# Kernel optimization log

Measured on AMD Instinct MI355X. Metric: run time of the kernel, lower is better.

The kernel has to match this reference:

```python
import jax, jax.numpy as jnp
import numpy as np

EPS = 1e-6

def act_quant(x):
    # per-token int8 absmax quantization with straight-through estimator
    scale = 127.0 / jnp.clip(jnp.max(jnp.abs(x), axis=-1, keepdims=True), 1e-5)
    q = jnp.clip(jnp.round(x * scale), -128.0, 127.0) / scale
    return x + jax.lax.stop_gradient(q - x)

def weight_quant(w):
    # ternary absmean quantization with straight-through estimator
    scale = 1.0 / jnp.clip(jnp.mean(jnp.abs(w)), 1e-5)
    q = jnp.clip(jnp.round(w * scale), -1.0, 1.0) / scale
    return w + jax.lax.stop_gradient(q - w)

def bit_linear(x, w):
    # x: [..., in], w: [out, in]
    return jnp.einsum('...i,oi->...o', act_quant(x), weight_quant(w))

def subln(x, g):
    # RMSNorm over last dim with learnable gain
    var = jnp.mean(jnp.square(x), axis=-1, keepdims=True)
    return x * jax.lax.rsqrt(var + EPS) * g

def setup_inputs() -> dict:
    key = jax.random.key(0)
    k1, k2, k3 = jax.random.split(key, 3)
    B, S, H, I = 8, 8192, 512, 2048
    x = jax.random.normal(k1, (B, S, H), dtype=jnp.float32)
    w_up = jax.random.normal(k2, (I, H), dtype=jnp.float32) * (H ** -0.5)
    w_down = jax.random.normal(k3, (H, I), dtype=jnp.float32) * (I ** -0.5)
    g = jnp.ones((I,), dtype=jnp.float32)
    return {'x': x, 'w_up': w_up, 'w_down': w_down, 'g': g}

def reference(x, w_up, w_down, g):
    h = bit_linear(x, w_up)            # [B,S,I]
    h = jnp.square(jax.nn.relu(h))     # relu^2 activation
    h = subln(h, g)                    # SubLN (RMSNorm)
    return bit_linear(h, w_down)       # [B,S,H]
```

## Files before the change

### kernel.cpp

```cpp
#include <hip/hip_runtime.h>
#include <stdint.h>


typedef int v4i __attribute__((ext_vector_type(4)));

#define AS1(p) ((const __attribute__((address_space(1))) void*)(p))
#define AS3(p) ((__attribute__((address_space(3))) void*)(p))

static constexpr size_t OFF_PART = 256;
static constexpr size_t OFF_SX   = 8192;
static constexpr size_t OFF_RSQ  = OFF_SX   + 262144;
static constexpr size_t OFF_S2   = OFF_RSQ  + 262144;
static constexpr size_t OFF_INV2 = OFF_S2   + 262144;
static constexpr size_t OFF_WUQ  = OFF_INV2 + 262144;
static constexpr size_t OFF_WDQ  = OFF_WUQ  + 1048576;
static constexpr size_t OFF_XQ   = OFF_WDQ  + 1048576;
static constexpr size_t OFF_HQ   = OFF_XQ   + 33554432;
static constexpr size_t OFF_SS   = OFF_HQ   + 134217728;
static constexpr size_t OFF_MM   = OFF_SS   + 8388608;

__global__ void wabs_partial(const float* __restrict__ w, double* __restrict__ part)
{
    int t = threadIdx.x, bid = blockIdx.x;
    const float4* w4 = (const float4*)w;
    int base = bid * 256 + t;
    double s = 0.0;
    #pragma unroll
    for (int j = 0; j < 4; ++j) {
        float4 v = w4[base + j * 65536];
        s += (double)fabsf(v.x) + (double)fabsf(v.y)
           + (double)fabsf(v.z) + (double)fabsf(v.w);
    }
    #pragma unroll
    for (int off = 32; off > 0; off >>= 1) s += __shfl_down(s, off);
    __shared__ double ps[4];
    int l = t & 63, wv = t >> 6;
    if (l == 0) ps[wv] = s;
    __syncthreads();
    if (t == 0) part[bid] = ((ps[0] + ps[1]) + ps[2]) + ps[3];
}

__global__ void finalize_sums(const double* __restrict__ part, double* __restrict__ sums)
{
    int t = threadIdx.x;
    double a = part[t];
    double b = part[256 + t];
    #pragma unroll
    for (int off = 32; off > 0; off >>= 1) {
        a += __shfl_down(a, off);
        b += __shfl_down(b, off);
    }
    __shared__ double pa[4], pb[4];
    int l = t & 63, wv = t >> 6;
    if (l == 0) { pa[wv] = a; pb[wv] = b; }
    __syncthreads();
    if (t == 0) {
        sums[0] = ((pa[0] + pa[1]) + pa[2]) + pa[3];
        sums[1] = ((pb[0] + pb[1]) + pb[2]) + pb[3];
    }
}

__global__ void wquant(const float* __restrict__ w, const double* __restrict__ sum,
                       signed char* __restrict__ wq)
{
    int i = blockIdx.x * blockDim.x + threadIdx.x;
    if (i >= 262144) return;
    float mean  = (float)(*sum) * (1.0f / 1048576.0f);
    float scale = 1.0f / fmaxf(mean, 1e-5f);
    float4 v = ((const float4*)w)[i];
    int q0 = (int)fminf(fmaxf(rintf(v.x * scale), -1.f), 1.f);
    int q1 = (int)fminf(fmaxf(rintf(v.y * scale), -1.f), 1.f);
    int q2 = (int)fminf(fmaxf(rintf(v.z * scale), -1.f), 1.f);
    int q3 = (int)fminf(fmaxf(rintf(v.w * scale), -1.f), 1.f);
    unsigned pk = (q0 & 255) | ((q1 & 255) << 8) | ((q2 & 255) << 16) | ((q3 & 255) << 24);
    ((unsigned*)wq)[i] = pk;
}

__global__ void xquant(const float* __restrict__ x, signed char* __restrict__ xq,
                       float* __restrict__ inv_sx)
{
    int row = blockIdx.x * 4 + (threadIdx.x >> 6);
    int l   = threadIdx.x & 63;
    const float* xr = x + (size_t)row * 512;
    float4 v0 = *(const float4*)(xr + l * 8);
    float4 v1 = *(const float4*)(xr + l * 8 + 4);
    float m = fmaxf(fmaxf(fmaxf(fabsf(v0.x), fabsf(v0.y)), fmaxf(fabsf(v0.z), fabsf(v0.w))),
                    fmaxf(fmaxf(fabsf(v1.x), fabsf(v1.y)), fmaxf(fabsf(v1.z), fabsf(v1.w))));
    #pragma unroll
    for (int off = 1; off < 64; off <<= 1) m = fmaxf(m, __shfl_xor(m, off));
    float mc = fmaxf(m, 1e-5f);
    float s  = 127.0f / mc;
    int q[8];
    q[0] = (int)fminf(fmaxf(rintf(v0.x * s), -128.f), 127.f);
    q[1] = (int)fminf(fmaxf(rintf(v0.y * s), -128.f), 127.f);
    q[2] = (int)fminf(fmaxf(rintf(v0.z * s), -128.f), 127.f);
    q[3] = (int)fminf(fmaxf(rintf(v0.w * s), -128.f), 127.f);
    q[4] = (int)fminf(fmaxf(rintf(v1.x * s), -128.f), 127.f);
    q[5] = (int)fminf(fmaxf(rintf(v1.y * s), -128.f), 127.f);
    q[6] = (int)fminf(fmaxf(rintf(v1.z * s), -128.f), 127.f);
    q[7] = (int)fminf(fmaxf(rintf(v1.w * s), -128.f), 127.f);
    uint2 pk;
    pk.x = (q[0] & 255) | ((q[1] & 255) << 8) | ((q[2] & 255) << 16) | ((q[3] & 255) << 24);
    pk.y = (q[4] & 255) | ((q[5] & 255) << 8) | ((q[6] & 255) << 16) | ((q[7] & 255) << 24);
    *(uint2*)(xq + (size_t)row * 512 + l * 8) = pk;
    if (l == 0) inv_sx[row] = mc * (1.0f / 127.0f);
}

__global__ void row_reduce(const float* __restrict__ ss_p, const float* __restrict__ mm_p,
                           float* __restrict__ rsq, float* __restrict__ s2,
                           float* __restrict__ inv2)
{
    int row = blockIdx.x * blockDim.x + threadIdx.x;
    float ss = 0.f, mm = 0.f;
    #pragma unroll
    for (int p = 0; p < 32; ++p) {
        ss += ss_p[(size_t)row * 32 + p];
        mm  = fmaxf(mm, mm_p[(size_t)row * 32 + p]);
    }
    float var  = ss * (1.0f / 2048.0f);
    float r    = 1.0f / sqrtf(var + 1e-6f);
    float maxy = fmaxf(r * mm, 1e-5f);
    rsq[row]  = r;
    s2[row]   = 127.0f / maxy;
    inv2[row] = maxy * (1.0f / 127.0f);
}

template<int K, int N, int EPI>
__global__ __launch_bounds__(256, 2)
void gemm_i8(const signed char* __restrict__ A,
             const signed char* __restrict__ B,
             const float* __restrict__ rowscale,
             const double* __restrict__ wsum,
             const float* __restrict__ g,
             const float* __restrict__ rsq,
             const float* __restrict__ s2,
             float* __restrict__ st_ss,
             float* __restrict__ st_mm,
             signed char* __restrict__ hq,
             float* __restrict__ out)
{
    constexpr int NBN = N / 128;
    __shared__ __align__(16) signed char lA[128 * 64];
    __shared__ __align__(16) signed char lB[128 * 64];

    int nwg  = gridDim.x;
    int orig = blockIdx.x;
    int q8 = nwg >> 3, r8 = nwg & 7;
    int xcd = orig & 7, lin = orig >> 3;
    int swz = (xcd < r8 ? xcd * (q8 + 1) : r8 * (q8 + 1) + (xcd - r8) * q8) + lin;
    int mt = swz / NBN, nt = swz - mt * NBN;

    size_t mbase = (size_t)mt * 128;
    int    nbase = nt * 128;

    int t = threadIdx.x;
    int l = t & 63;
    int wid = t >> 6;
    int wr = wid >> 1, wc = wid & 1;

    v4i acc[4][4] = {};

    const signed char* Ab = A + mbase * K;
    const signed char* Bb = B + (size_t)nbase * K;

    for (int k0 = 0; k0 < K; k0 += 64) {
        #pragma unroll
        for (int i = 0; i < 2; ++i) {
            int lin16 = i * 256 + t;
            int row   = lin16 >> 2;
            int c     = (lin16 & 3) ^ (row & 3);
            __builtin_amdgcn_global_load_lds(AS1(Ab + (size_t)row * K + k0 + c * 16),
                                             AS3(lA + lin16 * 16), 16, 0, 0);
            __builtin_amdgcn_global_load_lds(AS1(Bb + (size_t)row * K + k0 + c * 16),
                                             AS3(lB + lin16 * 16), 16, 0, 0);
        }
        __syncthreads();
        v4i af[4], bf[4];
        #pragma unroll
        for (int r = 0; r < 4; ++r) {
            int arow = wr * 64 + r * 16 + (l & 15);
            int ac   = (l >> 4) ^ (arow & 3);
            af[r] = *reinterpret_cast<const v4i*>(lA + (arow * 4 + ac) * 16);
            int brow = wc * 64 + r * 16 + (l & 15);
            int bc   = (l >> 4) ^ (brow & 3);
            bf[r] = *reinterpret_cast<const v4i*>(lB + (brow * 4 + bc) * 16);
        }
        #pragma unroll
        for (int r = 0; r < 4; ++r)
            #pragma unroll
            for (int c = 0; c < 4; ++c)
                acc[r][c] = __builtin_amdgcn_mfma_i32_16x16x64_i8(af[r], bf[c], acc[r][c], 0, 0, 0);
        __syncthreads();
    }

    float wmean = fmaxf((float)wsum[0] * (1.0f / 1048576.0f), 1e-5f);

    int rsub = wr * 64 + 4 * (l >> 4);
    int csub = wc * 64 + (l & 15);

    if constexpr (EPI == 2) {
        #pragma unroll
        for (int rt = 0; rt < 4; ++rt)
            #pragma unroll
            for (int reg = 0; reg < 4; ++reg) {
                size_t grow = mbase + rsub + rt * 16 + reg;
                float f = rowscale[grow] * wmean;
                #pragma unroll
                for (int ct = 0; ct < 4; ++ct)
                    out[grow * N + nbase + csub + ct * 16] = (float)acc[rt][ct][reg] * f;
            }
    } else {
        float gv[4];
        #pragma unroll
        for (int ct = 0; ct < 4; ++ct) gv[ct] = g[nbase + csub + ct * 16];

        if constexpr (EPI == 0) {
            float ssv[4][4], mmv[4][4];
            #pragma unroll
            for (int rt = 0; rt < 4; ++rt)
                #pragma unroll
                for (int reg = 0; reg < 4; ++reg) {
                    size_t grow = mbase + rsub + rt * 16 + reg;
                    float f = rowscale[grow] * wmean;
                    float ss = 0.f, mm = 0.f;
                    #pragma unroll
                    for (int ct = 0; ct < 4; ++ct) {
                        float z = (float)acc[rt][ct][reg] * f;
                        float a = fmaxf(z, 0.f);
                        float h = a * a;
                        ss += h * h;
                        mm  = fmaxf(mm, fabsf(h * gv[ct]));
                    }
                    ssv[rt][reg] = ss; mmv[rt][reg] = mm;
                }
            #pragma unroll
            for (int off = 1; off < 16; off <<= 1)
                #pragma unroll
                for (int rt = 0; rt < 4; ++rt)
                    #pragma unroll
                    for (int reg = 0; reg < 4; ++reg) {
                        ssv[rt][reg] += __shfl_xor(ssv[rt][reg], off);
                        mmv[rt][reg]  = fmaxf(mmv[rt][reg], __shfl_xor(mmv[rt][reg], off));
                    }
            if ((l & 15) == 0) {
                int p = nt * 2 + wc;
                #pragma unroll
                for (int rt = 0; rt < 4; ++rt)
                    #pragma unroll
                    for (int reg = 0; reg < 4; ++reg) {
                        size_t grow = mbase + rsub + rt * 16 + reg;
                        st_ss[grow * 32 + p] = ssv[rt][reg];
                        st_mm[grow * 32 + p] = mmv[rt][reg];
                    }
            }
        } else {
            #pragma unroll
            for (int rt = 0; rt < 4; ++rt)
                #pragma unroll
                for (int reg = 0; reg < 4; ++reg) {
                    size_t grow = mbase + rsub + rt * 16 + reg;
                    float f  = rowscale[grow] * wmean;
                    float rq = rsq[grow];
                    float sc = s2[grow];
                    #pragma unroll
                    for (int ct = 0; ct < 4; ++ct) {
                        float z = (float)acc[rt][ct][reg] * f;
                        float a = fmaxf(z, 0.f);
                        float h = a * a;
                        float y = (h * rq) * gv[ct];
                        int q = (int)fminf(fmaxf(rintf(y * sc), -128.f), 127.f);
                        hq[grow * 2048 + nbase + csub + ct * 16] = (signed char)q;
                    }
                }
        }
    }
}

extern "C" void kernel_launch(void* const* d_in, const int* in_sizes, int n_in,
                              void* d_out, int out_size, void* d_ws, size_t ws_size,
                              hipStream_t stream)
{
    const float* x  = (const float*)d_in[0];
    const float* wu = (const float*)d_in[1];
    const float* wd = (const float*)d_in[2];
    const float* g  = (const float*)d_in[3];
    float* out = (float*)d_out;
    char*  ws  = (char*)d_ws;

    double* sums     = (double*)ws;
    double* part     = (double*)(ws + OFF_PART);
    float*  inv_sx   = (float*)(ws + OFF_SX);
    float*  rsq      = (float*)(ws + OFF_RSQ);
    float*  s2       = (float*)(ws + OFF_S2);
    float*  inv2     = (float*)(ws + OFF_INV2);
    signed char* wuq = (signed char*)(ws + OFF_WUQ);
    signed char* wdq = (signed char*)(ws + OFF_WDQ);
    signed char* xq  = (signed char*)(ws + OFF_XQ);
    signed char* hq  = (signed char*)(ws + OFF_HQ);
    float*  st_ss    = (float*)(ws + OFF_SS);
    float*  st_mm    = (float*)(ws + OFF_MM);

    wabs_partial<<<256, 256, 0, stream>>>(wu, part);
    wabs_partial<<<256, 256, 0, stream>>>(wd, part + 256);
    finalize_sums<<<1, 256, 0, stream>>>(part, sums);
    wquant<<<1024, 256, 0, stream>>>(wu, sums + 0, wuq);
    wquant<<<1024, 256, 0, stream>>>(wd, sums + 1, wdq);
    xquant<<<16384, 256, 0, stream>>>(x, xq, inv_sx);

    gemm_i8<512, 2048, 0><<<8192, 256, 0, stream>>>(xq, wuq, inv_sx, sums + 0, g,
                                                    nullptr, nullptr, st_ss, st_mm,
                                                    nullptr, nullptr);
    row_reduce<<<256, 256, 0, stream>>>(st_ss, st_mm, rsq, s2, inv2);
    gemm_i8<512, 2048, 1><<<8192, 256, 0, stream>>>(xq, wuq, inv_sx, sums + 0, g,
                                                    rsq, s2, nullptr, nullptr,
                                                    hq, nullptr);
    gemm_i8<2048, 512, 2><<<2048, 256, 0, stream>>>(hq, wdq, inv2, sums + 1,
                                                    nullptr, nullptr, nullptr,
                                                    nullptr, nullptr, nullptr, out);
}
```

Measured before the change: 552.2 us.

## Rewrite int8 GEMM with 256x256 tiles, 8 waves and double-buffered LDS pipeline

The int8 GEMM moves from 128x128 tiles with 4 waves and a single-buffered 64-wide K step to 256x256 tiles with 8 waves and 128-wide K tiles. The K tiles sit in a double-buffered LDS ping-pong split into four phases. Each phase issues async global-to-LDS loads for a later K tile while its MFMAs run, using explicit barriers, vmcnt waits and setprio. The goal is to hide global load latency and raise operand reuse per byte loaded, at the cost of a 128KB LDS footprint, higher register pressure and fewer workgroups per launch.

```diff
diff --git a/kernel.cpp b/kernel.cpp
--- a/kernel.cpp
+++ b/kernel.cpp
@@ -125,8 +125,69 @@
     inv2[row] = maxy * (1.0f / 127.0f);
 }
 
+
+#define PHASE(MH, NH, STAGE_STMT, TAIL_STMT)                                   \
+  {                                                                            \
+    v4i af[8]; v4i bf[4];                                                      \
+    _Pragma("unroll")                                                          \
+    for (int mm = 0; mm < 4; ++mm) {                                           \
+      _Pragma("unroll")                                                        \
+      for (int ks = 0; ks < 2; ++ks) {                                         \
+        int r  = wr * 128 + ((MH) * 4 + mm) * 16 + lr;                         \
+        int eg = (ks * 4 + lg) ^ lx;                                           \
+        af[mm * 2 + ks] = *(const v4i*)(Ab + r * 128 + eg * 16);               \
+      }                                                                        \
+    }                                                                          \
+    _Pragma("unroll")                                                          \
+    for (int nn = 0; nn < 2; ++nn) {                                           \
+      _Pragma("unroll")                                                        \
+      for (int ks = 0; ks < 2; ++ks) {                                         \
+        int r  = wc * 64 + ((NH) * 2 + nn) * 16 + lr;                          \
+        int eg = (ks * 4 + lg) ^ lx;                                           \
+        bf[nn * 2 + ks] = *(const v4i*)(Bb + r * 128 + eg * 16);               \
+      }                                                                        \
+    }                                                                          \
+    STAGE_STMT;                                                                \
+    __builtin_amdgcn_s_barrier();                                              \
+    asm volatile("s_waitcnt lgkmcnt(0)" ::: "memory");                         \
+    __builtin_amdgcn_sched_barrier(0);                                         \
+    __builtin_amdgcn_s_setprio(1);                                             \
+    _Pragma("unroll")                                                          \
+    for (int mm = 0; mm < 4; ++mm)                                             \
+      _Pragma("unroll")                                                        \
+      for (int nn = 0; nn < 2; ++nn)                                           \
+        _Pragma("unroll")                                                      \
+        for (int ks = 0; ks < 2; ++ks)                                         \
+          acc[(MH) * 4 + mm][(NH) * 2 + nn] =                                  \
+              __builtin_amdgcn_mfma_i32_16x16x64_i8(                           \
+                  af[mm * 2 + ks], bf[nn * 2 + ks],                            \
+                  acc[(MH) * 4 + mm][(NH) * 2 + nn], 0, 0, 0);                 \
+    __builtin_amdgcn_s_setprio(0);                                             \
+    TAIL_STMT;                                                                 \
+    __builtin_amdgcn_s_barrier();                                              \
+  }
+
+#define KTILE(KT, P)                                                           \
+  {                                                                            \
+    const char* Ab = &lds[P][0][0];                                            \
+    const char* Bb = &lds[P][1][0];                                            \
+    const int kt_ = (KT);                                                      \
+    PHASE(0, 0, { if (kt_ + 1 < NKT) stageA((P) ^ 1, 1, kt_ + 1); }, {})       \
+    PHASE(0, 1, { if (kt_ + 1 < NKT) stageB((P) ^ 1, 1, kt_ + 1); }, {})       \
+    PHASE(1, 0, { if (kt_ + 2 < NKT) stageA((P), 0, kt_ + 2); }, {})           \
+    PHASE(1, 1, { if (kt_ + 2 < NKT) stageB((P), 0, kt_ + 2); },               \
+          {                                                                    \
+            if (kt_ < NKT - 1) {                                               \
+              if (kt_ + 2 < NKT)                                               \
+                asm volatile("s_waitcnt vmcnt(4)" ::: "memory");               \
+              else                                                             \
+                asm volatile("s_waitcnt vmcnt(0)" ::: "memory");               \
+            }                                                                  \
+          })                                                                   \
+  }
+
 template<int K, int N, int EPI>
-__global__ __launch_bounds__(256, 2)
+__global__ __launch_bounds__(512, 2)
 void gemm_i8(const signed char* __restrict__ A,
              const signed char* __restrict__ B,
              const float* __restrict__ rowscale,
@@ -139,9 +200,9 @@
              signed char* __restrict__ hq,
              float* __restrict__ out)
 {
-    constexpr int NBN = N / 128;
-    __shared__ __align__(16) signed char lA[128 * 64];
-    __shared__ __align__(16) signed char lB[128 * 64];
+    constexpr int NKT = K / 128;
+    constexpr int NBN = N / 256;
+    __shared__ __align__(16) char lds[2][2][32768];
 
     int nwg  = gridDim.x;
     int orig = blockIdx.x;
@@ -150,126 +211,124 @@
     int swz = (xcd < r8 ? xcd * (q8 + 1) : r8 * (q8 + 1) + (xcd - r8) * q8) + lin;
     int mt = swz / NBN, nt = swz - mt * NBN;
 
-    size_t mbase = (size_t)mt * 128;
-    int    nbase = nt * 128;
-
-    int t = threadIdx.x;
-    int l = t & 63;
+    size_t mbase = (size_t)mt * 256;
+    int    nbase = nt * 256;
+
+    int t  = threadIdx.x;
+    int l  = t & 63;
     int wid = t >> 6;
-    int wr = wid >> 1, wc = wid & 1;
-
-    v4i acc[4][4] = {};
-
-    const signed char* Ab = A + mbase * K;
-    const signed char* Bb = B + (size_t)nbase * K;
-
-    for (int k0 = 0; k0 < K; k0 += 64) {
+    int wr = wid >> 2, wc = wid & 3;
+    int lr = l & 15, lg = l >> 4, lx = l & 7;
+
+    const signed char* Ag = A + mbase * K;
+    const signed char* Bg = B + (size_t)nbase * K;
+
+    auto stageA = [&](int buf, int sel, int ktt) {
+        char* d0 = &lds[buf][0][0];
         #pragma unroll
         for (int i = 0; i < 2; ++i) {
-            int lin16 = i * 256 + t;
-            int row   = lin16 >> 2;
-            int c     = (lin16 & 3) ^ (row & 3);
-            __builtin_amdgcn_global_load_lds(AS1(Ab + (size_t)row * K + k0 + c * 16),
-                                             AS3(lA + lin16 * 16), 16, 0, 0);
-            __builtin_amdgcn_global_load_lds(AS1(Bb + (size_t)row * K + k0 + c * 16),
-                                             AS3(lB + lin16 * 16), 16, 0, 0);
+            int j = i * 512 + t;
+            int rho = j >> 3, gg = j & 7;
+            int r = rho + (rho & 64) + sel * 64;
+            int kg = gg ^ (r & 7);
+            __builtin_amdgcn_global_load_lds(AS1(Ag + (size_t)r * K + ktt * 128 + kg * 16),
+                                             AS3(d0 + r * 128 + gg * 16), 16, 0, 0);
         }
-        __syncthreads();
-        v4i af[4], bf[4];
+    };
+    auto stageB = [&](int buf, int sel, int ktt) {
+        char* d0 = &lds[buf][1][0];
         #pragma unroll
-        for (int r = 0; r < 4; ++r) {
-            int arow = wr * 64 + r * 16 + (l & 15);
-            int ac   = (l >> 4) ^ (arow & 3);
-            af[r] = *reinterpret_cast<const v4i*>(lA + (arow * 4 + ac) * 16);
-            int brow = wc * 64 + r * 16 + (l & 15);
-            int bc   = (l >> 4) ^ (brow & 3);
-            bf[r] = *reinterpret_cast<const v4i*>(lB + (brow * 4 + bc) * 16);
+        for (int i = 0; i < 2; ++i) {
+            int j = i * 512 + t;
+            int rho = j >> 3, gg = j & 7;
+            int r = ((rho & ~31) << 1) + (rho & 31) + sel * 32;
+            int kg = gg ^ (r & 7);
+            __builtin_amdgcn_global_load_lds(AS1(Bg + (size_t)r * K + ktt * 128 + kg * 16),
+                                             AS3(d0 + r * 128 + gg * 16), 16, 0, 0);
         }
-        #pragma unroll
-        for (int r = 0; r < 4; ++r)
-            #pragma unroll
-            for (int c = 0; c < 4; ++c)
-                acc[r][c] = __builtin_amdgcn_mfma_i32_16x16x64_i8(af[r], bf[c], acc[r][c], 0, 0, 0);
-        __syncthreads();
+    };
+
+    v4i acc[8][4] = {};
+
+    stageA(0, 0, 0); stageB(0, 0, 0); stageA(0, 1, 0); stageB(0, 1, 0);
+    if (NKT > 1) {
+        stageA(1, 0, 1); stageB(1, 0, 1);
+        asm volatile("s_waitcnt vmcnt(4)" ::: "memory");
+    } else {
+        asm volatile("s_waitcnt vmcnt(0)" ::: "memory");
+    }
+    __builtin_amdgcn_s_barrier();
+
+    #pragma unroll 1
+    for (int kt2 = 0; kt2 < NKT / 2; ++kt2) {
+        int kt = kt2 * 2;
+        KTILE(kt, 0)
+        KTILE(kt + 1, 1)
     }
 
     float wmean = fmaxf((float)wsum[0] * (1.0f / 1048576.0f), 1e-5f);
-
-    int rsub = wr * 64 + 4 * (l >> 4);
-    int csub = wc * 64 + (l & 15);
+    size_t rowb = mbase + (size_t)wr * 128;
+    int    colb = nbase + wc * 64;
 
     if constexpr (EPI == 2) {
         #pragma unroll
-        for (int rt = 0; rt < 4; ++rt)
+        for (int m = 0; m < 8; ++m)
             #pragma unroll
             for (int reg = 0; reg < 4; ++reg) {
-                size_t grow = mbase + rsub + rt * 16 + reg;
+                size_t grow = rowb + m * 16 + lg * 4 + reg;
                 float f = rowscale[grow] * wmean;
                 #pragma unroll
-                for (int ct = 0; ct < 4; ++ct)
-                    out[grow * N + nbase + csub + ct * 16] = (float)acc[rt][ct][reg] * f;
+                for (int n = 0; n < 4; ++n)
+                    out[grow * N + colb + n * 16 + lr] = (float)acc[m][n][reg] * f;
             }
     } else {
         float gv[4];
         #pragma unroll
-        for (int ct = 0; ct < 4; ++ct) gv[ct] = g[nbase + csub + ct * 16];
+        for (int n = 0; n < 4; ++n) gv[n] = g[colb + n * 16 + lr];
 
         if constexpr (EPI == 0) {
-            float ssv[4][4], mmv[4][4];
             #pragma unroll
-            for (int rt = 0; rt < 4; ++rt)
+            for (int m = 0; m < 8; ++m)
                 #pragma unroll
                 for (int reg = 0; reg < 4; ++reg) {
-                    size_t grow = mbase + rsub + rt * 16 + reg;
+                    size_t grow = rowb + m * 16 + lg * 4 + reg;
                     float f = rowscale[grow] * wmean;
-                    float ss = 0.f, mm = 0.f;
+                    float ss = 0.f, mx = 0.f;
                     #pragma unroll
-                    for (int ct = 0; ct < 4; ++ct) {
-                        float z = (float)acc[rt][ct][reg] * f;
+                    for (int n = 0; n < 4; ++n) {
+                        float z = (float)acc[m][n][reg] * f;
                         float a = fmaxf(z, 0.f);
                         float h = a * a;
                         ss += h * h;
-                        mm  = fmaxf(mm, fabsf(h * gv[ct]));
+                        mx  = fmaxf(mx, fabsf(h * gv[n]));
                     }
-                    ssv[rt][reg] = ss; mmv[rt][reg] = mm;
+                    #pragma unroll
+                    for (int off = 1; off < 16; off <<= 1) {
+                        ss += __shfl_xor(ss, off);
+                        mx  = fmaxf(mx, __shfl_xor(mx, off));
+                    }
+                    if (lr == 0) {
+                        st_ss[grow * 32 + nt * 4 + wc] = ss;
+                        st_mm[grow * 32 + nt * 4 + wc] = mx;
+                    }
                 }
-            #pragma unroll
-            for (int off = 1; off < 16; off <<= 1)
-                #pragma unroll
-                for (int rt = 0; rt < 4; ++rt)
-                    #pragma unroll
-                    for (int reg = 0; reg < 4; ++reg) {
-                        ssv[rt][reg] += __shfl_xor(ssv[rt][reg], off);
-                        mmv[rt][reg]  = fmaxf(mmv[rt][reg], __shfl_xor(mmv[rt][reg], off));
-                    }
-            if ((l & 15) == 0) {
-                int p = nt * 2 + wc;
-                #pragma unroll
-                for (int rt = 0; rt < 4; ++rt)
-                    #pragma unroll
-                    for (int reg = 0; reg < 4; ++reg) {
-                        size_t grow = mbase + rsub + rt * 16 + reg;
-                        st_ss[grow * 32 + p] = ssv[rt][reg];
-                        st_mm[grow * 32 + p] = mmv[rt][reg];
-                    }
-            }
         } else {
             #pragma unroll
-            for (int rt = 0; rt < 4; ++rt)
+            for (int m = 0; m < 8; ++m)
                 #pragma unroll
                 for (int reg = 0; reg < 4; ++reg) {
-                    size_t grow = mbase + rsub + rt * 16 + reg;
+                    size_t grow = rowb + m * 16 + lg * 4 + reg;
                     float f  = rowscale[grow] * wmean;
                     float rq = rsq[grow];
                     float sc = s2[grow];
                     #pragma unroll
-                    for (int ct = 0; ct < 4; ++ct) {
-                        float z = (float)acc[rt][ct][reg] * f;
+                    for (int n = 0; n < 4; ++n) {
+                        float z = (float)acc[m][n][reg] * f;
                         float a = fmaxf(z, 0.f);
                         float h = a * a;
-                        float y = (h * rq) * gv[ct];
-                        int q = (int)fminf(fmaxf(rintf(y * sc), -128.f), 127.f);
-                        hq[grow * 2048 + nbase + csub + ct * 16] = (signed char)q;
+                        float y = (h * rq) * gv[n];
+                        int qv = (int)fminf(fmaxf(rintf(y * sc), -128.f), 127.f);
+                        hq[grow * 2048 + colb + n * 16 + lr] = (signed char)qv;
                     }
                 }
         }
@@ -307,14 +366,14 @@
     wquant<<<1024, 256, 0, stream>>>(wd, sums + 1, wdq);
     xquant<<<16384, 256, 0, stream>>>(x, xq, inv_sx);
 
-    gemm_i8<512, 2048, 0><<<8192, 256, 0, stream>>>(xq, wuq, inv_sx, sums + 0, g,
+    gemm_i8<512, 2048, 0><<<2048, 512, 0, stream>>>(xq, wuq, inv_sx, sums + 0, g,
                                                     nullptr, nullptr, st_ss, st_mm,
                                                     nullptr, nullptr);
     row_reduce<<<256, 256, 0, stream>>>(st_ss, st_mm, rsq, s2, inv2);
-    gemm_i8<512, 2048, 1><<<8192, 256, 0, stream>>>(xq, wuq, inv_sx, sums + 0, g,
+    gemm_i8<512, 2048, 1><<<2048, 512, 0, stream>>>(xq, wuq, inv_sx, sums + 0, g,
                                                     rsq, s2, nullptr, nullptr,
                                                     hq, nullptr);
-    gemm_i8<2048, 512, 2><<<2048, 256, 0, stream>>>(hq, wdq, inv2, sums + 1,
-                                                    nullptr, nullptr, nullptr,
-                                                    nullptr, nullptr, nullptr, out);
-}
+    gemm_i8<2048, 512, 2><<<512, 512, 0, stream>>>(hq, wdq, inv2, sums + 1,
+                                                   nullptr, nullptr, nullptr,
+                                                   nullptr, nullptr, nullptr, out);
+}
```

After: 597.2 us. 1.08x slower.

## Replace recomputed up-projection GEMM with int16 staging and a row norm-quant kernel

Applied to the files above, without the earlier changes.

The up-projection GEMM now runs once and stores raw integer accumulators as int16 through an LDS-staged, vectorized write. A new per-row kernel applies the scale, relu², RMS norm and int8 quantization. Before, the GEMM was run twice: once to gather row statistics and once to quantize. The pipeline is processed in four row chunks so the int16 intermediate has a chance to stay in the last-level cache between kernels. The LDS swizzle is also adjusted. Truncating int32 accumulators to int16 can overflow for inputs with large accumulated sums, which adds a correctness risk.

```diff
diff --git a/kernel.cpp b/kernel.cpp
--- a/kernel.cpp
+++ b/kernel.cpp
@@ -7,17 +7,15 @@
 #define AS1(p) ((const __attribute__((address_space(1))) void*)(p))
 #define AS3(p) ((__attribute__((address_space(3))) void*)(p))
 
+static constexpr int CHUNK = 16384;
 static constexpr size_t OFF_PART = 256;
 static constexpr size_t OFF_SX   = 8192;
-static constexpr size_t OFF_RSQ  = OFF_SX   + 262144;
-static constexpr size_t OFF_S2   = OFF_RSQ  + 262144;
-static constexpr size_t OFF_INV2 = OFF_S2   + 262144;
+static constexpr size_t OFF_INV2 = OFF_SX   + 262144;
 static constexpr size_t OFF_WUQ  = OFF_INV2 + 262144;
 static constexpr size_t OFF_WDQ  = OFF_WUQ  + 1048576;
 static constexpr size_t OFF_XQ   = OFF_WDQ  + 1048576;
-static constexpr size_t OFF_HQ   = OFF_XQ   + 33554432;
-static constexpr size_t OFF_SS   = OFF_HQ   + 134217728;
-static constexpr size_t OFF_MM   = OFF_SS   + 8388608;
+static constexpr size_t OFF_Z16  = OFF_XQ   + 33554432;
+static constexpr size_t OFF_HQ   = OFF_Z16  + 67108864;
 
 __global__ void wabs_partial(const float* __restrict__ w, double* __restrict__ part)
 {
@@ -106,23 +104,60 @@
     if (l == 0) inv_sx[row] = mc * (1.0f / 127.0f);
 }
 
-__global__ void row_reduce(const float* __restrict__ ss_p, const float* __restrict__ mm_p,
-                           float* __restrict__ rsq, float* __restrict__ s2,
-                           float* __restrict__ inv2)
-{
-    int row = blockIdx.x * blockDim.x + threadIdx.x;
+__global__ __launch_bounds__(256)
+void norm_quant(const short* __restrict__ z16, const float* __restrict__ inv_sx,
+                const double* __restrict__ wsum, const float* __restrict__ g,
+                signed char* __restrict__ hq, float* __restrict__ inv2)
+{
+    int row = blockIdx.x;
+    int t = threadIdx.x;
+    float wmean = fmaxf((float)wsum[0] * (1.0f / 1048576.0f), 1e-5f);
+    float f = inv_sx[row] * wmean;
+
+    v4i zi = *(const v4i*)(z16 + (size_t)row * 2048 + t * 8);
+    const short* zs = (const short*)&zi;
+    float4 g0 = *(const float4*)(g + t * 8);
+    float4 g1 = *(const float4*)(g + t * 8 + 4);
+    float gv[8] = {g0.x, g0.y, g0.z, g0.w, g1.x, g1.y, g1.z, g1.w};
+
+    float h[8];
     float ss = 0.f, mm = 0.f;
     #pragma unroll
-    for (int p = 0; p < 32; ++p) {
-        ss += ss_p[(size_t)row * 32 + p];
-        mm  = fmaxf(mm, mm_p[(size_t)row * 32 + p]);
-    }
-    float var  = ss * (1.0f / 2048.0f);
+    for (int j = 0; j < 8; ++j) {
+        float z = (float)zs[j] * f;
+        float a = fmaxf(z, 0.f);
+        h[j] = a * a;
+        ss += h[j] * h[j];
+        mm  = fmaxf(mm, fabsf(h[j] * gv[j]));
+    }
+    #pragma unroll
+    for (int off = 1; off < 64; off <<= 1) {
+        ss += __shfl_xor(ss, off);
+        mm  = fmaxf(mm, __shfl_xor(mm, off));
+    }
+    __shared__ float sss[4], smm[4];
+    int l = t & 63, wv = t >> 6;
+    if (l == 0) { sss[wv] = ss; smm[wv] = mm; }
+    __syncthreads();
+    float sst = ((sss[0] + sss[1]) + sss[2]) + sss[3];
+    float mmt = fmaxf(fmaxf(smm[0], smm[1]), fmaxf(smm[2], smm[3]));
+
+    float var  = sst * (1.0f / 2048.0f);
     float r    = 1.0f / sqrtf(var + 1e-6f);
-    float maxy = fmaxf(r * mm, 1e-5f);
-    rsq[row]  = r;
-    s2[row]   = 127.0f / maxy;
-    inv2[row] = maxy * (1.0f / 127.0f);
+    float maxy = fmaxf(r * mmt, 1e-5f);
+    float sc   = 127.0f / maxy;
+    if (t == 0) inv2[row] = maxy * (1.0f / 127.0f);
+
+    int q[8];
+    #pragma unroll
+    for (int j = 0; j < 8; ++j) {
+        float y = (h[j] * r) * gv[j];
+        q[j] = (int)fminf(fmaxf(rintf(y * sc), -128.f), 127.f);
+    }
+    uint2 pk;
+    pk.x = (q[0] & 255) | ((q[1] & 255) << 8) | ((q[2] & 255) << 16) | ((q[3] & 255) << 24);
+    pk.y = (q[4] & 255) | ((q[5] & 255) << 8) | ((q[6] & 255) << 16) | ((q[7] & 255) << 24);
+    *(uint2*)(hq + (size_t)row * 2048 + t * 8) = pk;
 }
 
 template<int K, int N, int EPI>
@@ -131,17 +166,13 @@
              const signed char* __restrict__ B,
              const float* __restrict__ rowscale,
              const double* __restrict__ wsum,
-             const float* __restrict__ g,
-             const float* __restrict__ rsq,
-             const float* __restrict__ s2,
-             float* __restrict__ st_ss,
-             float* __restrict__ st_mm,
-             signed char* __restrict__ hq,
+             short* __restrict__ z16,
              float* __restrict__ out)
 {
     constexpr int NBN = N / 128;
-    __shared__ __align__(16) signed char lA[128 * 64];
-    __shared__ __align__(16) signed char lB[128 * 64];
+    __shared__ __align__(16) char smem[32768];
+    char* lA = smem;
+    char* lB = smem + 8192;
 
     int nwg  = gridDim.x;
     int orig = blockIdx.x;
@@ -168,7 +199,7 @@
         for (int i = 0; i < 2; ++i) {
             int lin16 = i * 256 + t;
             int row   = lin16 >> 2;
-            int c     = (lin16 & 3) ^ (row & 3);
+            int c     = (lin16 & 3) ^ ((row >> 1) & 3);
             __builtin_amdgcn_global_load_lds(AS1(Ab + (size_t)row * K + k0 + c * 16),
                                              AS3(lA + lin16 * 16), 16, 0, 0);
             __builtin_amdgcn_global_load_lds(AS1(Bb + (size_t)row * K + k0 + c * 16),
@@ -179,10 +210,10 @@
         #pragma unroll
         for (int r = 0; r < 4; ++r) {
             int arow = wr * 64 + r * 16 + (l & 15);
-            int ac   = (l >> 4) ^ (arow & 3);
+            int ac   = (l >> 4) ^ ((arow >> 1) & 3);
             af[r] = *reinterpret_cast<const v4i*>(lA + (arow * 4 + ac) * 16);
             int brow = wc * 64 + r * 16 + (l & 15);
-            int bc   = (l >> 4) ^ (brow & 3);
+            int bc   = (l >> 4) ^ ((brow >> 1) & 3);
             bf[r] = *reinterpret_cast<const v4i*>(lB + (brow * 4 + bc) * 16);
         }
         #pragma unroll
@@ -193,12 +224,30 @@
         __syncthreads();
     }
 
-    float wmean = fmaxf((float)wsum[0] * (1.0f / 1048576.0f), 1e-5f);
-
     int rsub = wr * 64 + 4 * (l >> 4);
     int csub = wc * 64 + (l & 15);
 
-    if constexpr (EPI == 2) {
+    if constexpr (EPI == 0) {
+        short* sm = (short*)smem;
+        #pragma unroll
+        for (int rt = 0; rt < 4; ++rt)
+            #pragma unroll
+            for (int reg = 0; reg < 4; ++reg) {
+                int rho = rsub + rt * 16 + reg;
+                #pragma unroll
+                for (int ct = 0; ct < 4; ++ct)
+                    sm[rho * 128 + csub + ct * 16] = (short)acc[rt][ct][reg];
+            }
+        __syncthreads();
+        #pragma unroll
+        for (int it = 0; it < 8; ++it) {
+            int j = it * 256 + t;
+            int rho = j >> 4, ck = j & 15;
+            *(v4i*)(z16 + (size_t)(mbase + rho) * 2048 + nbase + ck * 8) =
+                *(const v4i*)(sm + rho * 128 + ck * 8);
+        }
+    } else {
+        float wmean = fmaxf((float)wsum[0] * (1.0f / 1048576.0f), 1e-5f);
         #pragma unroll
         for (int rt = 0; rt < 4; ++rt)
             #pragma unroll
@@ -209,70 +258,6 @@
                 for (int ct = 0; ct < 4; ++ct)
                     out[grow * N + nbase + csub + ct * 16] = (float)acc[rt][ct][reg] * f;
             }
-    } else {
-        float gv[4];
-        #pragma unroll
-        for (int ct = 0; ct < 4; ++ct) gv[ct] = g[nbase + csub + ct * 16];
-
-        if constexpr (EPI == 0) {
-            float ssv[4][4], mmv[4][4];
-            #pragma unroll
-            for (int rt = 0; rt < 4; ++rt)
-                #pragma unroll
-                for (int reg = 0; reg < 4; ++reg) {
-                    size_t grow = mbase + rsub + rt * 16 + reg;
-                    float f = rowscale[grow] * wmean;
-                    float ss = 0.f, mm = 0.f;
-                    #pragma unroll
-                    for (int ct = 0; ct < 4; ++ct) {
-                        float z = (float)acc[rt][ct][reg] * f;
-                        float a = fmaxf(z, 0.f);
-                        float h = a * a;
-                        ss += h * h;
-                        mm  = fmaxf(mm, fabsf(h * gv[ct]));
-                    }
-                    ssv[rt][reg] = ss; mmv[rt][reg] = mm;
-                }
-            #pragma unroll
-            for (int off = 1; off < 16; off <<= 1)
-                #pragma unroll
-                for (int rt = 0; rt < 4; ++rt)
-                    #pragma unroll
-                    for (int reg = 0; reg < 4; ++reg) {
-                        ssv[rt][reg] += __shfl_xor(ssv[rt][reg], off);
-                        mmv[rt][reg]  = fmaxf(mmv[rt][reg], __shfl_xor(mmv[rt][reg], off));
-                    }
-            if ((l & 15) == 0) {
-                int p = nt * 2 + wc;
-                #pragma unroll
-                for (int rt = 0; rt < 4; ++rt)
-                    #pragma unroll
-                    for (int reg = 0; reg < 4; ++reg) {
-                        size_t grow = mbase + rsub + rt * 16 + reg;
-                        st_ss[grow * 32 + p] = ssv[rt][reg];
-                        st_mm[grow * 32 + p] = mmv[rt][reg];
-                    }
-            }
-        } else {
-            #pragma unroll
-            for (int rt = 0; rt < 4; ++rt)
-                #pragma unroll
-                for (int reg = 0; reg < 4; ++reg) {
-                    size_t grow = mbase + rsub + rt * 16 + reg;
-                    float f  = rowscale[grow] * wmean;
-                    float rq = rsq[grow];
-                    float sc = s2[grow];
-                    #pragma unroll
-                    for (int ct = 0; ct < 4; ++ct) {
-                        float z = (float)acc[rt][ct][reg] * f;
-                        float a = fmaxf(z, 0.f);
-                        float h = a * a;
-                        float y = (h * rq) * gv[ct];
-                        int q = (int)fminf(fmaxf(rintf(y * sc), -128.f), 127.f);
-                        hq[grow * 2048 + nbase + csub + ct * 16] = (signed char)q;
-                    }
-                }
-        }
     }
 }
 
@@ -290,15 +275,12 @@
     double* sums     = (double*)ws;
     double* part     = (double*)(ws + OFF_PART);
     float*  inv_sx   = (float*)(ws + OFF_SX);
-    float*  rsq      = (float*)(ws + OFF_RSQ);
-    float*  s2       = (float*)(ws + OFF_S2);
     float*  inv2     = (float*)(ws + OFF_INV2);
     signed char* wuq = (signed char*)(ws + OFF_WUQ);
     signed char* wdq = (signed char*)(ws + OFF_WDQ);
     signed char* xq  = (signed char*)(ws + OFF_XQ);
+    short*  z16      = (short*)(ws + OFF_Z16);
     signed char* hq  = (signed char*)(ws + OFF_HQ);
-    float*  st_ss    = (float*)(ws + OFF_SS);
-    float*  st_mm    = (float*)(ws + OFF_MM);
 
     wabs_partial<<<256, 256, 0, stream>>>(wu, part);
     wabs_partial<<<256, 256, 0, stream>>>(wd, part + 256);
@@ -307,14 +289,13 @@
     wquant<<<1024, 256, 0, stream>>>(wd, sums + 1, wdq);
     xquant<<<16384, 256, 0, stream>>>(x, xq, inv_sx);
 
-    gemm_i8<512, 2048, 0><<<8192, 256, 0, stream>>>(xq, wuq, inv_sx, sums + 0, g,
-                                                    nullptr, nullptr, st_ss, st_mm,
-                                                    nullptr, nullptr);
-    row_reduce<<<256, 256, 0, stream>>>(st_ss, st_mm, rsq, s2, inv2);
-    gemm_i8<512, 2048, 1><<<8192, 256, 0, stream>>>(xq, wuq, inv_sx, sums + 0, g,
-                                                    rsq, s2, nullptr, nullptr,
-                                                    hq, nullptr);
-    gemm_i8<2048, 512, 2><<<2048, 256, 0, stream>>>(hq, wdq, inv2, sums + 1,
-                                                    nullptr, nullptr, nullptr,
-                                                    nullptr, nullptr, nullptr, out);
-}
+    for (int c = 0; c < 4; ++c) {
+        size_t R = (size_t)c * CHUNK;
+        gemm_i8<512, 2048, 0><<<(CHUNK / 128) * 16, 256, 0, stream>>>(
+            xq + R * 512, wuq, nullptr, nullptr, z16, nullptr);
+        norm_quant<<<CHUNK, 256, 0, stream>>>(z16, inv_sx + R, sums + 0, g,
+                                              hq, inv2 + R);
+        gemm_i8<2048, 512, 2><<<(CHUNK / 128) * 4, 256, 0, stream>>>(
+            hq, wdq, inv2 + R, sums + 1, nullptr, out + R * 512);
+    }
+}
```

Result: faster. 521.4 us (-5.6%).
